# Performance work log

Hardware: AMD Instinct MI355X
Metric: run time of the kernel (lower is better)

Reference implementation:

```python
import jax, jax.numpy as jnp
import numpy as np

NUM_HEADS = 12


def _attend(q, k, v, scale):
    # q: [B,H,Q,D], k/v: [B,H,K,D]
    attn = jnp.einsum('bhqd,bhkd->bhqk', q, k) * scale
    attn = jax.nn.softmax(attn, axis=-1)
    return jnp.einsum('bhqk,bhkd->bhqd', attn, v)


def setup_inputs() -> dict:
    key = jax.random.key(0)
    k1, k2, k3 = jax.random.split(key, 3)
    B, N, C = 32, 1009, 768
    x = jax.random.normal(k1, (B, N, C), dtype=jnp.float32)
    W_qkv = jax.random.normal(k2, (C, 3 * C), dtype=jnp.float32) * (C ** -0.5)
    b_qkv = jnp.zeros((3 * C,), dtype=jnp.float32)
    W_proj = jax.random.normal(k3, (C, C), dtype=jnp.float32) * (C ** -0.5)
    b_proj = jnp.zeros((C,), dtype=jnp.float32)
    return {"x": x, "W_qkv": W_qkv, "b_qkv": b_qkv, "W_proj": W_proj,
            "b_proj": b_proj, "query_len": 1, "lens_z": 432}


def reference(x, W_qkv, b_qkv, W_proj, b_proj, query_len, lens_z):
    B, N, C = x.shape
    H = NUM_HEADS
    D = C // H
    scale = D ** -0.5
    lens_x = N - query_len - lens_z

    qkv = (x @ W_qkv + b_qkv).reshape(B, N, 3, H, D)
    qkv = jnp.transpose(qkv, (2, 0, 3, 1, 4))  # [3,B,H,N,D]
    q, k, v = qkv[0], qkv[1], qkv[2]

    sl_p = slice(0, query_len)
    sl_t = slice(query_len, query_len + lens_z)
    sl_s = slice(query_len + lens_z, N)

    # prompt: local self-attention
    x_prompt = _attend(q[:, :, sl_p], k[:, :, sl_p], v[:, :, sl_p], scale)
    # template: local self-attention
    x_template = _attend(q[:, :, sl_t], k[:, :, sl_t], v[:, :, sl_t], scale)
    # search: global attention over all tokens
    x_search = _attend(q[:, :, sl_s], k, v, scale)

    def merge(y, L):
        return jnp.transpose(y, (0, 2, 1, 3)).reshape(B, L, C)

    out = jnp.concatenate([merge(x_prompt, query_len),
                           merge(x_template, lens_z),
                           merge(x_search, lens_x)], axis=1)
    return out @ W_proj + b_proj
```

## Files before the change

kernel.cpp:

```cpp
#include <hip/hip_runtime.h>

#define B_ 32
#define N_ 1009
#define C_ 768
#define H_ 12
#define D_ 64
#define M_ (B_*N_)
#define MT_ 253
#define MPAD_ (MT_*128)
#define NKV_ 1024

typedef __attribute__((ext_vector_type(4))) float f32x4;
typedef __attribute__((ext_vector_type(8))) short s16x8;

__device__ __forceinline__ unsigned short f2bf(float f) {
  union { float f; unsigned u; } x; x.f = f;
  unsigned r = x.u + 0x7fffu + ((x.u >> 16) & 1u);
  return (unsigned short)(r >> 16);
}

__device__ __forceinline__ f32x4 mfma16(s16x8 a, s16x8 b, f32x4 c) {
  return __builtin_amdgcn_mfma_f32_16x16x32_bf16(a, b, c, 0, 0, 0);
}

__device__ __forceinline__ void async16(const void* g, void* l) {
  __builtin_amdgcn_global_load_lds((const __attribute__((address_space(1))) void*)g,
                                   (__attribute__((address_space(3))) void*)l, 16, 0, 0);
}

__device__ __forceinline__ float exp2_fast(float x) {
  float r; asm("v_exp_f32 %0, %1" : "=v"(r) : "v"(x)); return r;
}

__device__ __forceinline__ unsigned cvt_pk_bf16(float lo, float hi) {
  unsigned r; asm("v_cvt_pk_bf16_f32 %0, %1, %2" : "=v"(r) : "v"(lo), "v"(hi)); return r;
}

template<int NWG>
__device__ __forceinline__ int xcd_swz(int bid) {
  constexpr int q = NWG >> 3, r = NWG & 7;
  const int x = bid & 7, l = bid >> 3;
  return (x < r ? x * (q + 1) : r * (q + 1) + (x - r) * q) + l;
}

__global__ void convert_x(const float* __restrict__ x, unsigned short* __restrict__ xb) {
  const long e = ((long)blockIdx.x * 256 + threadIdx.x) * 8;
  const long row = e / 768;
  s16x8 v;
  if (row < M_) {
#pragma unroll
    for (int j = 0; j < 8; ++j) v[j] = (short)f2bf(x[e + j]);
  } else {
    v = (s16x8){0,0,0,0,0,0,0,0};
  }
  *(s16x8*)&xb[e] = v;
}

__global__ void transpose_convert(const float* __restrict__ in, unsigned short* __restrict__ out,
                                  int R, int Ccols) {
  __shared__ float tile[64][65];
  const int tc = blockIdx.x * 64, tr = blockIdx.y * 64;
#pragma unroll
  for (int i = 0; i < 16; ++i) {
    const int e = i * 256 + threadIdx.x;
    const int r = e >> 6, c = e & 63;
    tile[r][c] = in[(long)(tr + r) * Ccols + tc + c];
  }
  __syncthreads();
#pragma unroll
  for (int i = 0; i < 16; ++i) {
    const int e = i * 256 + threadIdx.x;
    const int c = e >> 6, r = e & 63;
    out[(long)(tc + c) * R + tr + r] = f2bf(tile[r][c]);
  }
}

__global__ void zero_pad(unsigned short* __restrict__ kb, unsigned short* __restrict__ vt) {
  const int t = blockIdx.x * 256 + threadIdx.x;
  if (t >= 368640) return;
  const int d = t & 63;
  const int r = t >> 6;
  const int bh = r / 15, tok = 1009 + (r - bh * 15);
  kb[(((long)bh << 10) + tok) * 64 + d] = 0;
  const int c = t % 15, row = t / 15;
  vt[((long)row << 10) + 1009 + c] = 0;
}

template<int MODE>
__global__ __launch_bounds__(256, 4)
void gemm_bt(const unsigned short* __restrict__ A,
             const unsigned short* __restrict__ Bt,
             const float* __restrict__ bias,
             unsigned short* __restrict__ qo,
             unsigned short* __restrict__ ko,
             unsigned short* __restrict__ vo,
             float* __restrict__ fo) {
  __shared__ __align__(16) unsigned short smem[17408];
  const int tid = threadIdx.x;
  const int lane = tid & 63;
  const int wv = tid >> 6;
  constexpr int NBN = (MODE == 0) ? 18 : 6;
  const int swzid = xcd_swz<MT_ * NBN>(blockIdx.x);
  const int bm = swzid / NBN;
  const int bn = swzid - bm * NBN;
  const int row0 = bm * 128;
  const int col0 = bn * 128;
  const int wr = (wv >> 1) * 64;
  const int wc = (wv & 1) * 64;

  auto stage = [&](int bufsel, int kt) {
#pragma unroll
    for (int c = 0; c < 2; ++c) {
      const int lds_off = c * 4096 + wv * 1024;
      const int gg = c * 256 + wv * 64 + lane;
      const int row = gg >> 2;
      const int ck = ((gg & 3) ^ ((row >> 1) & 3)) << 3;
      async16(A + (long)(row0 + row) * 768 + kt + ck, (char*)smem + bufsel * 8192 + lds_off);
      async16(Bt + (long)(col0 + row) * 768 + kt + ck, (char*)smem + 16384 + bufsel * 8192 + lds_off);
    }
  };

  f32x4 acc[4][4] = {};
  stage(0, 0);
  for (int it = 0; it < 24; ++it) {
    const int buf = it & 1;
    if (it + 1 < 24) {
      stage(buf ^ 1, (it + 1) * 32);
      asm volatile("s_waitcnt vmcnt(4)" ::: "memory");
    } else {
      asm volatile("s_waitcnt vmcnt(0)" ::: "memory");
    }
    __builtin_amdgcn_s_barrier();

    const unsigned short* Asb = smem + buf * 4096;
    const unsigned short* Bsb = smem + 8192 + buf * 4096;
    s16x8 af[4], bfr[4];
#pragma unroll
    for (int m = 0; m < 4; ++m) {
      const int rA = wr + m * 16 + (lane & 15);
      af[m] = *(const s16x8*)&Asb[rA * 32 + (((lane >> 4) ^ ((rA >> 1) & 3)) << 3)];
    }
#pragma unroll
    for (int n = 0; n < 4; ++n) {
      const int rB = wc + n * 16 + (lane & 15);
      bfr[n] = *(const s16x8*)&Bsb[rB * 32 + (((lane >> 4) ^ ((rB >> 1) & 3)) << 3)];
    }
    __builtin_amdgcn_s_setprio(1);
#pragma unroll
    for (int m = 0; m < 4; ++m)
#pragma unroll
      for (int n = 0; n < 4; ++n)
        acc[m][n] = mfma16(af[m], bfr[n], acc[m][n]);
    __builtin_amdgcn_s_setprio(0);

    asm volatile("s_waitcnt lgkmcnt(0)" ::: "memory");
    __builtin_amdgcn_s_barrier();
  }

  if (MODE == 0 && col0 >= 1536) {
#pragma unroll
    for (int m = 0; m < 4; ++m)
#pragma unroll
      for (int j = 0; j < 4; ++j)
#pragma unroll
        for (int n = 0; n < 4; ++n) {
          const int dl = wc + n * 16 + (lane & 15);
          const int tk = wr + m * 16 + (lane >> 4) * 4 + j;
          smem[dl * 136 + tk] = f2bf(acc[m][n][j] + bias[col0 + dl]);
        }
    __syncthreads();
    const int h0 = (col0 - 1536) >> 6;
    const int b0 = row0 / N_;
    const int split = (b0 + 1) * N_ - row0;
#pragma unroll
    for (int it = 0; it < 8; ++it) {
      const int g = it * 256 + tid;
      const int dl = g >> 4;
      const int t8 = (g & 15) * 8;
      const s16x8 vv = *(const s16x8*)&smem[dl * 136 + t8];
      const int hh = h0 + (dl >> 6), dd = dl & 63;
#pragma unroll
      for (int jj = 0; jj < 8; ++jj) {
        const int tkb = t8 + jj;
        const int grow = row0 + tkb;
        if (grow < M_) {
          const int bb = (tkb < split) ? b0 : b0 + 1;
          const int ntok = grow - bb * N_;
          vo[(((((long)bb * H_ + hh) << 6) + dd) << 10) + ntok] = (unsigned short)vv[jj];
        }
      }
    }
    return;
  }

#pragma unroll
  for (int m = 0; m < 4; ++m) {
#pragma unroll
    for (int j = 0; j < 4; ++j) {
      const int grow = row0 + wr + m * 16 + (lane >> 4) * 4 + j;
      if (grow < M_) {
        if (MODE == 0) {
          const int b = grow / N_;
          const int ntok = grow - b * N_;
#pragma unroll
          for (int n = 0; n < 4; ++n) {
            const int col = col0 + wc + n * 16 + (lane & 15);
            float val = acc[m][n][j] + bias[col];
            const int which = col >= 768;
            if (!which) val *= 0.18033688011112042f;
            const int rem = col - which * 768;
            const int h = rem >> 6, d = rem & 63;
            const long bh = (long)b * H_ + h;
            unsigned short* dst = which ? ko : qo;
            dst[((bh << 10) + ntok) * 64 + d] = f2bf(val);
          }
        } else {
#pragma unroll
          for (int n = 0; n < 4; ++n) {
            const int col = col0 + wc + n * 16 + (lane & 15);
            fo[(long)grow * 768 + col] = acc[m][n][j] + bias[col];
          }
        }
      }
    }
  }
}

__global__ void misc_copy(const unsigned short* __restrict__ vt, unsigned short* __restrict__ og) {
  const int t = blockIdx.x * 256 + threadIdx.x;
  if (t >= B_ * H_ * D_) return;
  const int d = t & 63;
  const int bh = t >> 6;
  const int b = bh / H_, h = bh - b * H_;
  og[((long)b * N_) * 768 + h * 64 + d] = vt[(((long)bh << 6) + d) << 10];
}

__global__ __launch_bounds__(256, 4)
void attn_kernel(const unsigned short* __restrict__ qg,
                 const unsigned short* __restrict__ kg,
                 const unsigned short* __restrict__ vtg,
                 unsigned short* __restrict__ og) {
  __shared__ __align__(16) unsigned short Ks[2][64 * 64];
  __shared__ __align__(16) unsigned short Vts[2][64 * 64];
  __shared__ __align__(16) unsigned short Ps[64 * 64];

  const int bid = blockIdx.x;
  const int swz = (bid & 7) * 768 + (bid >> 3);
  const int tile = swz & 15;
  const int bh = swz >> 4;
  const int b = bh / H_;
  const int h = bh - b * H_;
  int qbase, qend, kstart, ktiles, kend;
  if (tile < 7) { qbase = 1 + 64 * tile;       qend = 433;  kstart = 1; ktiles = 7;  kend = 433; }
  else          { qbase = 433 + 64 * (tile-7); qend = 1009; kstart = 0; ktiles = 16; kend = 1009; }
  const long base  = (long)bh << 10;
  const long vbase = (long)bh << 6;
  const int tid = threadIdx.x, lane = tid & 63, wv = tid >> 6;
  const int q15 = lane & 15, q7 = lane & 7, g = lane >> 4;

  s16x8 qa[2];
  {
    const unsigned short* qp = qg + (base + qbase + wv * 16 + q15) * 64;
    qa[0] = *(const s16x8*)(qp + g * 8);
    qa[1] = *(const s16x8*)(qp + 32 + g * 8);
  }
  asm volatile("s_waitcnt vmcnt(0)" ::: "memory");

  f32x4 o[4] = {};
  float mrow = -1e30f, lrow = 0.f;

  auto stage = [&](int bufsel, int kb0) {
#pragma unroll
    for (int it = 0; it < 2; ++it) {
      const int ldsoff = (it * 256 + wv * 64) * 16;
      const int gr = it * 256 + wv * 64 + lane;
      const int rl = gr >> 3;
      const int cs = (gr & 7) ^ (rl & 7);
      async16(kg + ((base + kb0 + rl) << 6) + cs * 8, (char*)&Ks[bufsel][0] + ldsoff);
      async16(vtg + ((vbase + rl) << 10) + kb0 + cs * 8, (char*)&Vts[bufsel][0] + ldsoff);
    }
  };

  const int prow = wv * 16 + q15;

  stage(0, kstart);
  for (int kt = 0; kt < ktiles; ++kt) {
    const int buf = kt & 1;
    const int kbase0 = kstart + 64 * kt;
    if (kt + 1 < ktiles) {
      stage(buf ^ 1, kbase0 + 64);
      asm volatile("s_waitcnt vmcnt(4)" ::: "memory");
    } else {
      asm volatile("s_waitcnt vmcnt(0)" ::: "memory");
    }
    __builtin_amdgcn_s_barrier();

    f32x4 s4[4];
    __builtin_amdgcn_s_setprio(1);
#pragma unroll
    for (int n = 0; n < 4; ++n) {
      const int krow = n * 16 + q15;
      const int r7 = krow & 7;
      f32x4 a = {};
      a = mfma16(*(const s16x8*)&Ks[buf][krow * 64 + ((g ^ r7) << 3)],       qa[0], a);
      a = mfma16(*(const s16x8*)&Ks[buf][krow * 64 + (((4 + g) ^ r7) << 3)], qa[1], a);
      s4[n] = a;
    }
    __builtin_amdgcn_s_setprio(0);

    if (kbase0 + 64 > kend) {
#pragma unroll
      for (int n = 0; n < 4; ++n)
#pragma unroll
        for (int j = 0; j < 4; ++j)
          if (kbase0 + n * 16 + g * 4 + j >= kend) s4[n][j] = -1e30f;
    }

    float rmax = fmaxf(
        fmaxf(fmaxf(fmaxf(s4[0][0], s4[0][1]), fmaxf(s4[0][2], s4[0][3])),
              fmaxf(fmaxf(s4[1][0], s4[1][1]), fmaxf(s4[1][2], s4[1][3]))),
        fmaxf(fmaxf(fmaxf(s4[2][0], s4[2][1]), fmaxf(s4[2][2], s4[2][3])),
              fmaxf(fmaxf(s4[3][0], s4[3][1]), fmaxf(s4[3][2], s4[3][3]))));
    rmax = fmaxf(rmax, __shfl_xor(rmax, 16));
    rmax = fmaxf(rmax, __shfl_xor(rmax, 32));

    const float mnew = fmaxf(mrow, rmax);
    const float corr = exp2_fast(mrow - mnew);
    mrow = mnew;
#pragma unroll
    for (int f = 0; f < 4; ++f)
#pragma unroll
      for (int j = 0; j < 4; ++j) o[f][j] *= corr;

    float psum = 0.f;
#pragma unroll
    for (int n = 0; n < 4; ++n) {
#pragma unroll
      for (int j = 0; j < 4; ++j) {
        s4[n][j] = exp2_fast(s4[n][j] - mnew);
        psum += s4[n][j];
      }
      uint2 pw;
      pw.x = cvt_pk_bf16(s4[n][0], s4[n][1]);
      pw.y = cvt_pk_bf16(s4[n][2], s4[n][3]);
      *(uint2*)((char*)Ps + prow * 128 + (((n * 2 + (g >> 1)) ^ q7) << 4) + (g & 1) * 8) = pw;
    }
    psum += __shfl_xor(psum, 16);
    psum += __shfl_xor(psum, 32);
    lrow = lrow * corr + psum;

    s16x8 pa[2];
#pragma unroll
    for (int kf = 0; kf < 2; ++kf)
      pa[kf] = *(const s16x8*)((char*)Ps + prow * 128 + (((kf * 4 + g) ^ q7) << 4));
    __builtin_amdgcn_s_setprio(1);
#pragma unroll
    for (int f = 0; f < 4; ++f) {
      const int vrow = f * 16 + q15;
      const int v7 = vrow & 7;
#pragma unroll
      for (int kf = 0; kf < 2; ++kf) {
        const s16x8 vb = *(const s16x8*)&Vts[buf][vrow * 64 + (((kf * 4 + g) ^ v7) << 3)];
        o[f] = mfma16(vb, pa[kf], o[f]);
      }
    }
    __builtin_amdgcn_s_setprio(0);

    asm volatile("s_waitcnt lgkmcnt(0)" ::: "memory");
    __builtin_amdgcn_s_barrier();
  }

  const int qrow = qbase + wv * 16 + q15;
  if (qrow < qend) {
    const float inv = 1.0f / lrow;
    unsigned short* op = og + ((long)b * N_ + qrow) * 768 + h * 64 + g * 4;
#pragma unroll
    for (int f = 0; f < 4; ++f) {
      uint2 ow;
      ow.x = cvt_pk_bf16(o[f][0] * inv, o[f][1] * inv);
      ow.y = cvt_pk_bf16(o[f][2] * inv, o[f][3] * inv);
      *(uint2*)(op + f * 16) = ow;
    }
  }
}

extern "C" void kernel_launch(void* const* d_in, const int* in_sizes, int n_in,
                              void* d_out, int out_size, void* d_ws, size_t ws_size,
                              hipStream_t stream) {
  const float* x      = (const float*)d_in[0];
  const float* W_qkv  = (const float*)d_in[1];
  const float* b_qkv  = (const float*)d_in[2];
  const float* W_proj = (const float*)d_in[3];
  const float* b_proj = (const float*)d_in[4];
  float* out = (float*)d_out;

  unsigned short* ws = (unsigned short*)d_ws;
  unsigned short* wqkvT  = ws;
  unsigned short* wprojT = wqkvT + (long)2304 * 768;
  unsigned short* qb = wprojT + (long)768 * 768;
  const long kvsz = (long)B_ * H_ * NKV_ * D_;
  unsigned short* kb = qb + kvsz;
  unsigned short* vb = kb + kvsz;
  unsigned short* xb = vb + kvsz;
  unsigned short* attnout = xb;

  zero_pad<<<1440, 256, 0, stream>>>(kb, vb);
  convert_x<<<12144, 256, 0, stream>>>(x, xb);
  transpose_convert<<<dim3(2304 / 64, 768 / 64), 256, 0, stream>>>(W_qkv, wqkvT, 768, 2304);
  transpose_convert<<<dim3(768 / 64, 768 / 64), 256, 0, stream>>>(W_proj, wprojT, 768, 768);
  gemm_bt<0><<<MT_ * 18, 256, 0, stream>>>(xb, wqkvT, b_qkv, qb, kb, vb, nullptr);
  misc_copy<<<96, 256, 0, stream>>>(vb, attnout);
  attn_kernel<<<B_ * H_ * 16, 256, 0, stream>>>(qb, kb, vb, attnout);
  gemm_bt<1><<<MT_ * 6, 256, 0, stream>>>(attnout, wprojT, b_proj, nullptr, nullptr, nullptr, out);
}
```

Measured before the change: 413.9 us.

## Use 256x256 tiles with 4-stage async pipeline for QKV GEMM

Replaces the shared 128x128 GEMM for the QKV projection with a dedicated 512-thread kernel that computes 256x256 output tiles. It uses a 4-slot LDS ring with three K-steps prefetched ahead, and interleaves the A and B staging between two MFMA half-phases. The larger tile raises arithmetic intensity and cuts redundant global loads of x and W. It also uses 128 KB of LDS per block, which lowers occupancy, and the V-transpose epilogue now runs in two passes. Rows past the padded M are clamped so out-of-range loads stay in bounds.

```diff
diff --git a/kernel.cpp b/kernel.cpp
--- a/kernel.cpp
+++ b/kernel.cpp
@@ -9,6 +9,7 @@
 #define MT_ 253
 #define MPAD_ (MT_*128)
 #define NKV_ 1024
+#define MT2_ 127
 
 typedef __attribute__((ext_vector_type(4))) float f32x4;
 typedef __attribute__((ext_vector_type(8))) short s16x8;
@@ -86,23 +87,189 @@
   vt[((long)row << 10) + 1009 + c] = 0;
 }
 
-template<int MODE>
+__global__ __launch_bounds__(512, 2)
+void gemm_qkv(const unsigned short* __restrict__ A,
+              const unsigned short* __restrict__ Bt,
+              const float* __restrict__ bias,
+              unsigned short* __restrict__ qo,
+              unsigned short* __restrict__ ko,
+              unsigned short* __restrict__ vo) {
+  __shared__ __align__(16) unsigned short smem[65536];
+  const int tid = threadIdx.x;
+  const int lane = tid & 63;
+  const int wv = tid >> 6;
+  const int swzid = xcd_swz<MT2_ * 9>(blockIdx.x);
+  const int bm = swzid / 9;
+  const int bn = swzid - bm * 9;
+  const int row0 = bm * 256;
+  const int col0 = bn * 256;
+  const int wr = (wv >> 2) * 128;
+  const int wc = (wv & 3) * 64;
+  const int l15 = lane & 15, g4 = lane >> 4;
+
+  const unsigned short* pa[2];
+  const unsigned short* pb[2];
+#pragma unroll
+  for (int s = 0; s < 2; ++s) {
+    const int gg = s * 512 + tid;
+    const int row = gg >> 2;
+    const int ck = ((gg & 3) ^ ((row >> 1) & 3)) << 3;
+    int rowA = row0 + row;
+    if (rowA >= MPAD_) rowA -= 128;
+    pa[s] = A + (long)rowA * 768 + ck;
+    pb[s] = Bt + (long)(col0 + row) * 768 + ck;
+  }
+
+  auto stage_op = [&](int slot, int koff, int which) {
+#pragma unroll
+    for (int s = 0; s < 2; ++s) {
+      const int ldsb = slot * 32768 + which * 16384 + s * 8192 + wv * 1024;
+      async16((which ? pb[s] : pa[s]) + koff, (char*)smem + ldsb);
+    }
+  };
+
+  f32x4 acc[8][4] = {};
+
+#pragma unroll
+  for (int t0 = 0; t0 < 3; ++t0) {
+    stage_op(t0, t0 * 32, 0);
+    stage_op(t0, t0 * 32, 1);
+  }
+  asm volatile("s_waitcnt vmcnt(8)" ::: "memory");
+  __builtin_amdgcn_s_barrier();
+
+  for (int t = 0; t < 24; ++t) {
+    const int sl = t & 3;
+    const unsigned short* As = smem + sl * 16384;
+    const unsigned short* Bs = As + 8192;
+    const bool st = (t + 3) < 24;
+    const int s3 = (t + 3) & 3;
+    const int koff3 = (t + 3) * 32;
+
+    s16x8 af[4], bf[4];
+#pragma unroll
+    for (int m = 0; m < 4; ++m) {
+      const int rA = wr + m * 16 + l15;
+      af[m] = *(const s16x8*)&As[rA * 32 + ((g4 ^ ((rA >> 1) & 3)) << 3)];
+    }
+#pragma unroll
+    for (int n = 0; n < 4; ++n) {
+      const int rB = wc + n * 16 + l15;
+      bf[n] = *(const s16x8*)&Bs[rB * 32 + ((g4 ^ ((rB >> 1) & 3)) << 3)];
+    }
+    if (st) stage_op(s3, koff3, 0);
+    __builtin_amdgcn_s_barrier();
+    asm volatile("s_waitcnt lgkmcnt(0)" ::: "memory");
+    __builtin_amdgcn_s_setprio(1);
+#pragma unroll
+    for (int m = 0; m < 4; ++m)
+#pragma unroll
+      for (int n = 0; n < 4; ++n)
+        acc[m][n] = mfma16(af[m], bf[n], acc[m][n]);
+    __builtin_amdgcn_s_setprio(0);
+    __builtin_amdgcn_s_barrier();
+
+#pragma unroll
+    for (int m = 0; m < 4; ++m) {
+      const int rA = wr + (m + 4) * 16 + l15;
+      af[m] = *(const s16x8*)&As[rA * 32 + ((g4 ^ ((rA >> 1) & 3)) << 3)];
+    }
+    if (st) stage_op(s3, koff3, 1);
+    __builtin_amdgcn_s_barrier();
+    asm volatile("s_waitcnt lgkmcnt(0)" ::: "memory");
+    __builtin_amdgcn_s_setprio(1);
+#pragma unroll
+    for (int m = 0; m < 4; ++m)
+#pragma unroll
+      for (int n = 0; n < 4; ++n)
+        acc[m + 4][n] = mfma16(af[m], bf[n], acc[m + 4][n]);
+    __builtin_amdgcn_s_setprio(0);
+
+    if (t <= 20)      asm volatile("s_waitcnt vmcnt(8)" ::: "memory");
+    else if (t == 21) asm volatile("s_waitcnt vmcnt(4)" ::: "memory");
+    else if (t == 22) asm volatile("s_waitcnt vmcnt(0)" ::: "memory");
+    __builtin_amdgcn_s_barrier();
+  }
+
+  if (col0 >= 1536) {
+    const int h0 = (col0 - 1536) >> 6;
+    const int b0 = row0 / N_;
+    const int split = (b0 + 1) * N_ - row0;
+#pragma unroll
+    for (int pass = 0; pass < 2; ++pass) {
+      __syncthreads();
+      if ((wv >> 2) == pass) {
+#pragma unroll
+        for (int m = 0; m < 8; ++m)
+#pragma unroll
+          for (int j = 0; j < 4; ++j)
+#pragma unroll
+            for (int n = 0; n < 4; ++n) {
+              const int dl = wc + n * 16 + l15;
+              const int tk = m * 16 + g4 * 4 + j;
+              smem[dl * 136 + tk] = f2bf(acc[m][n][j] + bias[col0 + dl]);
+            }
+      }
+      __syncthreads();
+      const int tb = pass * 128;
+#pragma unroll
+      for (int it = 0; it < 8; ++it) {
+        const int gg2 = it * 512 + tid;
+        const int dl = gg2 >> 4;
+        const int t8 = (gg2 & 15) * 8;
+        const s16x8 vv = *(const s16x8*)&smem[dl * 136 + t8];
+        const int hh = h0 + (dl >> 6), dd = dl & 63;
+#pragma unroll
+        for (int jj = 0; jj < 8; ++jj) {
+          const int tkb = tb + t8 + jj;
+          const int grw = row0 + tkb;
+          if (grw < M_) {
+            const int bb = (tkb < split) ? b0 : b0 + 1;
+            const int ntok = grw - bb * N_;
+            vo[(((((long)bb * H_ + hh) << 6) + dd) << 10) + ntok] = (unsigned short)vv[jj];
+          }
+        }
+      }
+    }
+    return;
+  }
+
+  const int which = col0 >= 768;
+#pragma unroll
+  for (int m = 0; m < 8; ++m) {
+#pragma unroll
+    for (int j = 0; j < 4; ++j) {
+      const int grw = row0 + wr + m * 16 + g4 * 4 + j;
+      if (grw < M_) {
+        const int b = grw / N_;
+        const int ntok = grw - b * N_;
+#pragma unroll
+        for (int n = 0; n < 4; ++n) {
+          const int col = col0 + wc + n * 16 + l15;
+          float val = acc[m][n][j] + bias[col];
+          if (!which) val *= 0.18033688011112042f;
+          const int rem = col - which * 768;
+          const int h = rem >> 6, d = rem & 63;
+          const long bh2 = (long)b * H_ + h;
+          (which ? ko : qo)[((bh2 << 10) + ntok) * 64 + d] = f2bf(val);
+        }
+      }
+    }
+  }
+}
+
 __global__ __launch_bounds__(256, 4)
-void gemm_bt(const unsigned short* __restrict__ A,
-             const unsigned short* __restrict__ Bt,
-             const float* __restrict__ bias,
-             unsigned short* __restrict__ qo,
-             unsigned short* __restrict__ ko,
-             unsigned short* __restrict__ vo,
-             float* __restrict__ fo) {
+void gemm_proj(const unsigned short* __restrict__ A,
+               const unsigned short* __restrict__ Bt,
+               const float* __restrict__ bias,
+               float* __restrict__ fo) {
   __shared__ __align__(16) unsigned short smem[17408];
   const int tid = threadIdx.x;
   const int lane = tid & 63;
   const int wv = tid >> 6;
-  constexpr int NBN = (MODE == 0) ? 18 : 6;
-  const int swzid = xcd_swz<MT_ * NBN>(blockIdx.x);
-  const int bm = swzid / NBN;
-  const int bn = swzid - bm * NBN;
+  const int swzid = xcd_swz<MT_ * 6>(blockIdx.x);
+  const int bm = swzid / 6;
+  const int bn = swzid - bm * 6;
   const int row0 = bm * 128;
   const int col0 = bn * 128;
   const int wr = (wv >> 1) * 64;
@@ -157,69 +324,16 @@
     __builtin_amdgcn_s_barrier();
   }
 
-  if (MODE == 0 && col0 >= 1536) {
-#pragma unroll
-    for (int m = 0; m < 4; ++m)
-#pragma unroll
-      for (int j = 0; j < 4; ++j)
-#pragma unroll
-        for (int n = 0; n < 4; ++n) {
-          const int dl = wc + n * 16 + (lane & 15);
-          const int tk = wr + m * 16 + (lane >> 4) * 4 + j;
-          smem[dl * 136 + tk] = f2bf(acc[m][n][j] + bias[col0 + dl]);
-        }
-    __syncthreads();
-    const int h0 = (col0 - 1536) >> 6;
-    const int b0 = row0 / N_;
-    const int split = (b0 + 1) * N_ - row0;
-#pragma unroll
-    for (int it = 0; it < 8; ++it) {
-      const int g = it * 256 + tid;
-      const int dl = g >> 4;
-      const int t8 = (g & 15) * 8;
-      const s16x8 vv = *(const s16x8*)&smem[dl * 136 + t8];
-      const int hh = h0 + (dl >> 6), dd = dl & 63;
-#pragma unroll
-      for (int jj = 0; jj < 8; ++jj) {
-        const int tkb = t8 + jj;
-        const int grow = row0 + tkb;
-        if (grow < M_) {
-          const int bb = (tkb < split) ? b0 : b0 + 1;
-          const int ntok = grow - bb * N_;
-          vo[(((((long)bb * H_ + hh) << 6) + dd) << 10) + ntok] = (unsigned short)vv[jj];
-        }
-      }
-    }
-    return;
-  }
-
 #pragma unroll
   for (int m = 0; m < 4; ++m) {
 #pragma unroll
     for (int j = 0; j < 4; ++j) {
       const int grow = row0 + wr + m * 16 + (lane >> 4) * 4 + j;
       if (grow < M_) {
-        if (MODE == 0) {
-          const int b = grow / N_;
-          const int ntok = grow - b * N_;
-#pragma unroll
-          for (int n = 0; n < 4; ++n) {
-            const int col = col0 + wc + n * 16 + (lane & 15);
-            float val = acc[m][n][j] + bias[col];
-            const int which = col >= 768;
-            if (!which) val *= 0.18033688011112042f;
-            const int rem = col - which * 768;
-            const int h = rem >> 6, d = rem & 63;
-            const long bh = (long)b * H_ + h;
-            unsigned short* dst = which ? ko : qo;
-            dst[((bh << 10) + ntok) * 64 + d] = f2bf(val);
-          }
-        } else {
-#pragma unroll
-          for (int n = 0; n < 4; ++n) {
-            const int col = col0 + wc + n * 16 + (lane & 15);
-            fo[(long)grow * 768 + col] = acc[m][n][j] + bias[col];
-          }
+#pragma unroll
+        for (int n = 0; n < 4; ++n) {
+          const int col = col0 + wc + n * 16 + (lane & 15);
+          fo[(long)grow * 768 + col] = acc[m][n][j] + bias[col];
         }
       }
     }
@@ -408,8 +522,8 @@
   convert_x<<<12144, 256, 0, stream>>>(x, xb);
   transpose_convert<<<dim3(2304 / 64, 768 / 64), 256, 0, stream>>>(W_qkv, wqkvT, 768, 2304);
   transpose_convert<<<dim3(768 / 64, 768 / 64), 256, 0, stream>>>(W_proj, wprojT, 768, 768);
-  gemm_bt<0><<<MT_ * 18, 256, 0, stream>>>(xb, wqkvT, b_qkv, qb, kb, vb, nullptr);
+  gemm_qkv<<<MT2_ * 9, 512, 0, stream>>>(xb, wqkvT, b_qkv, qb, kb, vb);
   misc_copy<<<96, 256, 0, stream>>>(vb, attnout);
   attn_kernel<<<B_ * H_ * 16, 256, 0, stream>>>(qb, kb, vb, attnout);
-  gemm_bt<1><<<MT_ * 6, 256, 0, stream>>>(attnout, wprojT, b_proj, nullptr, nullptr, nullptr, out);
-}
+  gemm_proj<<<MT_ * 6, 256, 0, stream>>>(attnout, wprojT, b_proj, out);
+}
```

Measured after the change: 419.6 us. No clear change (+1.4%).
